# Performance work log

Measured on AMD Instinct MI355X. Metric: run time of the kernel, lower is better.

## Reference

```python
import jax, jax.numpy as jnp
import numpy as np

LAMBDA_COORD = 5.0
LAMBDA_NOOBJ = 0.5
GRID = 7
IMG = 448.0
CELL = IMG / GRID  # 64.0
EPS = 1e-06


def setup_inputs() -> dict:
    key = jax.random.key(0)
    k1, k2, k3 = jax.random.split(key, 3)
    B = 16384
    # predictions in [0.05, 1) so sqrt(w), sqrt(h) are well-behaved (as in training)
    input_ = jax.random.uniform(k1, (B, 30, GRID, GRID), dtype=jnp.float32, minval=0.05, maxval=1.0)
    target = jax.random.uniform(k2, (B, GRID, GRID, 30), dtype=jnp.float32, minval=0.05, maxval=1.0)
    # objectness target must be exactly 1.0 for 'has object' cells (code tests == 1)
    has_obj = (jax.random.uniform(k3, (B, GRID, GRID)) > 0.7).astype(jnp.float32)
    target = target.at[:, :, :, 4].set(has_obj)
    return {"input_": input_, "target": target}


def _corners(rows30, col, row):
    # rows30: [N,30] cell-relative preds; col/row: [N] grid indices
    # returns x1,y1,x2,y2 each [N,2] (two boxes per cell), clipped to image
    cx = rows30[:, jnp.array([0, 5])] * CELL + (col * CELL)[:, None]
    cy = rows30[:, jnp.array([1, 6])] * CELL + (row * CELL)[:, None]
    w = rows30[:, jnp.array([2, 7])] * IMG
    h = rows30[:, jnp.array([3, 8])] * IMG
    x1 = jnp.clip(cx - w / 2, 0.0, IMG)
    y1 = jnp.clip(cy - h / 2, 0.0, IMG)
    x2 = jnp.clip(cx + w / 2, 0.0, IMG)
    y2 = jnp.clip(cy + h / 2, 0.0, IMG)
    return x1, y1, x2, y2


def _yolo_loss(input_, target):
    B = input_.shape[0]
    # [B,30,7,7] -> [B,7,7,30] -> [N,30]
    x = jnp.transpose(input_, (0, 2, 3, 1)).reshape(-1, 30)
    t = target.reshape(-1, 30)
    N = x.shape[0]

    # grid offsets: flat index = b*49 + row*7 + col
    cell_idx = jnp.arange(GRID * GRID)
    col = jnp.tile((cell_idx % GRID).astype(x.dtype), B)  # [N]
    row = jnp.tile((cell_idx // GRID).astype(x.dtype), B)  # [N]

    ix1, iy1, ix2, iy2 = _corners(x, col, row)
    tx1, ty1, tx2, ty2 = _corners(t, col, row)

    # IoU of each predicted box vs same-slot target box, [N,2]
    iw = jnp.maximum(jnp.minimum(ix2, tx2) - jnp.maximum(ix1, tx1), EPS)
    ih = jnp.maximum(jnp.minimum(iy2, ty2) - jnp.maximum(iy1, ty1), EPS)
    inter = iw * ih
    area_sum = (ix2 - ix1) * (iy2 - iy1) + (tx2 - tx1) * (ty2 - ty1)
    iou2 = inter / (area_sum - inter)  # [N,2]

    m = iou2[:, 0] < iou2[:, 1]                       # box 1 selected where True
    iou = jnp.where(m, iou2[:, 1], iou2[:, 0])        # [N]

    has_obj = (t[:, 4] == 1.0).astype(x.dtype)        # [N]
    no_obj = 1.0 - has_obj

    sel = jnp.where(m[:, None], x[:, 5:10], x[:, :5])  # [N,5] selected box

    coordinate_error = jnp.sum(has_obj * ((sel[:, 0] - t[:, 0]) ** 2 + (sel[:, 1] - t[:, 1]) ** 2))
    size_error = jnp.sum(has_obj * ((jnp.sqrt(sel[:, 2]) - jnp.sqrt(t[:, 2])) ** 2
                                    + (jnp.sqrt(sel[:, 3]) - jnp.sqrt(t[:, 3])) ** 2))
    confidence_error = jnp.sum(has_obj * (sel[:, 4] - iou) ** 2)
    classification_error = jnp.sum(has_obj[:, None] * (x[:, 10:] - t[:, 10:]) ** 2)
    noobj_confidence_error = jnp.sum(no_obj * (x[:, 4] ** 2 + x[:, 9] ** 2))

    loss = (LAMBDA_COORD * coordinate_error + LAMBDA_COORD * size_error
            + confidence_error + LAMBDA_NOOBJ * noobj_confidence_error
            + classification_error)
    return loss / B


def reference(input_, target):
    return _yolo_loss(input_, target)
```

## Files before the change

kernel.cpp:

```cpp
#include <hip/hip_runtime.h>


#define CELLF   64.0f
#define IMGF    448.0f
#define EPSF    1e-6f
#define LAMBDA_COORD 5.0f
#define LAMBDA_NOOBJ 0.5f

__global__ __launch_bounds__(256) void yolo_loss_kernel(
    const float* __restrict__ input,
    const float* __restrict__ target,
    float* __restrict__ out,
    int ncells, float inv_b)
{
    __shared__ float s_t[256 * 30];
    __shared__ float s_part[4];

    const int tid  = threadIdx.x;
    const int base = blockIdx.x * 256;
    const int cells_here = min(256, ncells - base);

    if (cells_here == 256) {
        const float4* tg4 = reinterpret_cast<const float4*>(target + (size_t)base * 30);
        float4* s4 = reinterpret_cast<float4*>(s_t);
        #pragma unroll
        for (int i = 0; i < 8; ++i) {
            int idx = tid + i * 256;
            if (idx < 1920) s4[idx] = tg4[idx];
        }
    } else {
        int nflt = cells_here * 30;
        for (int i = tid; i < nflt; i += 256)
            s_t[i] = target[(size_t)base * 30 + i];
    }
    __syncthreads();

    float lv = 0.0f;
    const int n = base + tid;
    if (tid < cells_here) {
        const int b    = n / 49;
        const int cell = n - b * 49;
        const int row  = cell / 7;
        const int col  = cell - row * 7;

        const float* xin = input + (size_t)b * 1470 + cell;
        float x[30];
        #pragma unroll
        for (int c = 0; c < 30; ++c) x[c] = xin[c * 49];

        const float* t = s_t + tid * 30;

        const float colf = (float)col * CELLF;
        const float rowf = (float)row * CELLF;

        float iou[2];
        #pragma unroll
        for (int k = 0; k < 2; ++k) {
            const int o = 5 * k;
            float pcx = x[o + 0] * CELLF + colf;
            float pcy = x[o + 1] * CELLF + rowf;
            float pw  = x[o + 2] * IMGF;
            float ph  = x[o + 3] * IMGF;
            float px1 = fminf(fmaxf(pcx - 0.5f * pw, 0.0f), IMGF);
            float py1 = fminf(fmaxf(pcy - 0.5f * ph, 0.0f), IMGF);
            float px2 = fminf(fmaxf(pcx + 0.5f * pw, 0.0f), IMGF);
            float py2 = fminf(fmaxf(pcy + 0.5f * ph, 0.0f), IMGF);

            float tcx = t[o + 0] * CELLF + colf;
            float tcy = t[o + 1] * CELLF + rowf;
            float tw  = t[o + 2] * IMGF;
            float th  = t[o + 3] * IMGF;
            float tx1 = fminf(fmaxf(tcx - 0.5f * tw, 0.0f), IMGF);
            float ty1 = fminf(fmaxf(tcy - 0.5f * th, 0.0f), IMGF);
            float tx2 = fminf(fmaxf(tcx + 0.5f * tw, 0.0f), IMGF);
            float ty2 = fminf(fmaxf(tcy + 0.5f * th, 0.0f), IMGF);

            float iw = fmaxf(fminf(px2, tx2) - fmaxf(px1, tx1), EPSF);
            float ih = fmaxf(fminf(py2, ty2) - fmaxf(py1, ty1), EPSF);
            float inter = iw * ih;
            float area  = (px2 - px1) * (py2 - py1) + (tx2 - tx1) * (ty2 - ty1);
            iou[k] = inter / (area - inter);
        }

        const bool  m      = iou[0] < iou[1];
        const float iouSel = m ? iou[1] : iou[0];
        const float has_obj = (t[4] == 1.0f) ? 1.0f : 0.0f;
        const float no_obj  = 1.0f - has_obj;

        const float s0 = m ? x[5] : x[0];
        const float s1 = m ? x[6] : x[1];
        const float s2 = m ? x[7] : x[2];
        const float s3 = m ? x[8] : x[3];
        const float s4 = m ? x[9] : x[4];

        float d0 = s0 - t[0], d1 = s1 - t[1];
        float coord_e = d0 * d0 + d1 * d1;

        float e2 = sqrtf(s2) - sqrtf(t[2]);
        float e3 = sqrtf(s3) - sqrtf(t[3]);
        float size_e = e2 * e2 + e3 * e3;

        float dc = s4 - iouSel;
        float conf_e = dc * dc;

        float cls_e = 0.0f;
        #pragma unroll
        for (int c = 10; c < 30; ++c) {
            float d = x[c] - t[c];
            cls_e += d * d;
        }

        float noobj_e = x[4] * x[4] + x[9] * x[9];

        lv = has_obj * (LAMBDA_COORD * coord_e + LAMBDA_COORD * size_e + conf_e + cls_e)
           + LAMBDA_NOOBJ * no_obj * noobj_e;
    }

    float v = lv;
    #pragma unroll
    for (int off = 32; off > 0; off >>= 1)
        v += __shfl_down(v, off, 64);

    if ((tid & 63) == 0) s_part[tid >> 6] = v;
    __syncthreads();

    if (tid == 0) {
        float tot = s_part[0] + s_part[1] + s_part[2] + s_part[3];
        atomicAdd(out, tot * inv_b);
    }
}

extern "C" void kernel_launch(void* const* d_in, const int* in_sizes, int n_in,
                              void* d_out, int out_size, void* d_ws, size_t ws_size,
                              hipStream_t stream) {
    const float* input  = (const float*)d_in[0];
    const float* target = (const float*)d_in[1];
    float* out = (float*)d_out;

    const int B = in_sizes[0] / (30 * 49);
    const int ncells = B * 49;
    const int nblocks = (ncells + 255) / 256;

    hipMemsetAsync(out, 0, sizeof(float) * out_size, stream);
    yolo_loss_kernel<<<nblocks, 256, 0, stream>>>(input, target, out, ncells,
                                                  1.0f / (float)B);
}
```

Before: 207.6 us.

## Drop LDS target staging, process two cells per thread, two-pass reduction

```diff
diff --git a/kernel.cpp b/kernel.cpp
--- a/kernel.cpp
+++ b/kernel.cpp
@@ -7,127 +7,149 @@
 #define LAMBDA_COORD 5.0f
 #define LAMBDA_NOOBJ 0.5f
 
-__global__ __launch_bounds__(256) void yolo_loss_kernel(
+#define TPB 256
+#define CPT 2
+#define CPB (TPB * CPT)
+
+__device__ __forceinline__ float cell_loss(const float* __restrict__ input,
+                                           const float* __restrict__ target,
+                                           int n)
+{
+    const int b    = n / 49;
+    const int cell = n - b * 49;
+    const int row  = cell / 7;
+    const int col  = cell - row * 7;
+
+    const float* xin = input + (size_t)b * 1470 + cell;
+    float x[30];
+    #pragma unroll
+    for (int c = 0; c < 30; ++c) x[c] = xin[c * 49];
+
+    const float2* tp = reinterpret_cast<const float2*>(target + (size_t)n * 30);
+    float t[30];
+    #pragma unroll
+    for (int j = 0; j < 15; ++j) {
+        float2 v = tp[j];
+        t[2 * j]     = v.x;
+        t[2 * j + 1] = v.y;
+    }
+
+    const float colf = (float)col * CELLF;
+    const float rowf = (float)row * CELLF;
+
+    float iou[2];
+    #pragma unroll
+    for (int k = 0; k < 2; ++k) {
+        const int o = 5 * k;
+        float pcx = x[o + 0] * CELLF + colf;
+        float pcy = x[o + 1] * CELLF + rowf;
+        float pw  = x[o + 2] * IMGF;
+        float ph  = x[o + 3] * IMGF;
+        float px1 = fminf(fmaxf(pcx - 0.5f * pw, 0.0f), IMGF);
+        float py1 = fminf(fmaxf(pcy - 0.5f * ph, 0.0f), IMGF);
+        float px2 = fminf(fmaxf(pcx + 0.5f * pw, 0.0f), IMGF);
+        float py2 = fminf(fmaxf(pcy + 0.5f * ph, 0.0f), IMGF);
+
+        float tcx = t[o + 0] * CELLF + colf;
+        float tcy = t[o + 1] * CELLF + rowf;
+        float tw  = t[o + 2] * IMGF;
+        float th  = t[o + 3] * IMGF;
+        float tx1 = fminf(fmaxf(tcx - 0.5f * tw, 0.0f), IMGF);
+        float ty1 = fminf(fmaxf(tcy - 0.5f * th, 0.0f), IMGF);
+        float tx2 = fminf(fmaxf(tcx + 0.5f * tw, 0.0f), IMGF);
+        float ty2 = fminf(fmaxf(tcy + 0.5f * th, 0.0f), IMGF);
+
+        float iw = fmaxf(fminf(px2, tx2) - fmaxf(px1, tx1), EPSF);
+        float ih = fmaxf(fminf(py2, ty2) - fmaxf(py1, ty1), EPSF);
+        float inter = iw * ih;
+        float area  = (px2 - px1) * (py2 - py1) + (tx2 - tx1) * (ty2 - ty1);
+        iou[k] = inter / (area - inter);
+    }
+
+    const bool  m      = iou[0] < iou[1];
+    const float iouSel = m ? iou[1] : iou[0];
+    const float has_obj = (t[4] == 1.0f) ? 1.0f : 0.0f;
+    const float no_obj  = 1.0f - has_obj;
+
+    const float s0 = m ? x[5] : x[0];
+    const float s1 = m ? x[6] : x[1];
+    const float s2 = m ? x[7] : x[2];
+    const float s3 = m ? x[8] : x[3];
+    const float s4 = m ? x[9] : x[4];
+
+    float d0 = s0 - t[0], d1 = s1 - t[1];
+    float coord_e = d0 * d0 + d1 * d1;
+
+    float e2 = sqrtf(s2) - sqrtf(t[2]);
+    float e3 = sqrtf(s3) - sqrtf(t[3]);
+    float size_e = e2 * e2 + e3 * e3;
+
+    float dc = s4 - iouSel;
+    float conf_e = dc * dc;
+
+    float cls_e = 0.0f;
+    #pragma unroll
+    for (int c = 10; c < 30; ++c) {
+        float d = x[c] - t[c];
+        cls_e += d * d;
+    }
+
+    float noobj_e = x[4] * x[4] + x[9] * x[9];
+
+    return has_obj * (LAMBDA_COORD * coord_e + LAMBDA_COORD * size_e + conf_e + cls_e)
+         + LAMBDA_NOOBJ * no_obj * noobj_e;
+}
+
+__global__ __launch_bounds__(TPB) void yolo_main(
     const float* __restrict__ input,
     const float* __restrict__ target,
-    float* __restrict__ out,
-    int ncells, float inv_b)
+    float* __restrict__ partial,
+    int ncells)
 {
-    __shared__ float s_t[256 * 30];
-    __shared__ float s_part[4];
+    const int tid  = threadIdx.x;
+    const int base = blockIdx.x * CPB;
 
-    const int tid  = threadIdx.x;
-    const int base = blockIdx.x * 256;
-    const int cells_here = min(256, ncells - base);
+    float acc = 0.0f;
+    #pragma unroll
+    for (int it = 0; it < CPT; ++it) {
+        const int n = base + it * TPB + tid;
+        if (n < ncells) acc += cell_loss(input, target, n);
+    }
 
-    if (cells_here == 256) {
-        const float4* tg4 = reinterpret_cast<const float4*>(target + (size_t)base * 30);
-        float4* s4 = reinterpret_cast<float4*>(s_t);
-        #pragma unroll
-        for (int i = 0; i < 8; ++i) {
-            int idx = tid + i * 256;
-            if (idx < 1920) s4[idx] = tg4[idx];
-        }
-    } else {
-        int nflt = cells_here * 30;
-        for (int i = tid; i < nflt; i += 256)
-            s_t[i] = target[(size_t)base * 30 + i];
-    }
+    #pragma unroll
+    for (int off = 32; off > 0; off >>= 1)
+        acc += __shfl_down(acc, off, 64);
+
+    __shared__ float s_part[TPB / 64];
+    if ((tid & 63) == 0) s_part[tid >> 6] = acc;
     __syncthreads();
 
-    float lv = 0.0f;
-    const int n = base + tid;
-    if (tid < cells_here) {
-        const int b    = n / 49;
-        const int cell = n - b * 49;
-        const int row  = cell / 7;
-        const int col  = cell - row * 7;
+    if (tid == 0) {
+        float tot = 0.0f;
+        #pragma unroll
+        for (int w = 0; w < TPB / 64; ++w) tot += s_part[w];
+        partial[blockIdx.x] = tot;
+    }
+}
 
-        const float* xin = input + (size_t)b * 1470 + cell;
-        float x[30];
-        #pragma unroll
-        for (int c = 0; c < 30; ++c) x[c] = xin[c * 49];
+__global__ __launch_bounds__(256) void yolo_reduce(
+    const float* __restrict__ partial, int nparts,
+    float* __restrict__ out, float inv_b)
+{
+    const int tid = threadIdx.x;
+    float v = 0.0f;
+    for (int i = tid; i < nparts; i += 256) v += partial[i];
 
-        const float* t = s_t + tid * 30;
-
-        const float colf = (float)col * CELLF;
-        const float rowf = (float)row * CELLF;
-
-        float iou[2];
-        #pragma unroll
-        for (int k = 0; k < 2; ++k) {
-            const int o = 5 * k;
-            float pcx = x[o + 0] * CELLF + colf;
-            float pcy = x[o + 1] * CELLF + rowf;
-            float pw  = x[o + 2] * IMGF;
-            float ph  = x[o + 3] * IMGF;
-            float px1 = fminf(fmaxf(pcx - 0.5f * pw, 0.0f), IMGF);
-            float py1 = fminf(fmaxf(pcy - 0.5f * ph, 0.0f), IMGF);
-            float px2 = fminf(fmaxf(pcx + 0.5f * pw, 0.0f), IMGF);
-            float py2 = fminf(fmaxf(pcy + 0.5f * ph, 0.0f), IMGF);
-
-            float tcx = t[o + 0] * CELLF + colf;
-            float tcy = t[o + 1] * CELLF + rowf;
-            float tw  = t[o + 2] * IMGF;
-            float th  = t[o + 3] * IMGF;
-            float tx1 = fminf(fmaxf(tcx - 0.5f * tw, 0.0f), IMGF);
-            float ty1 = fminf(fmaxf(tcy - 0.5f * th, 0.0f), IMGF);
-            float tx2 = fminf(fmaxf(tcx + 0.5f * tw, 0.0f), IMGF);
-            float ty2 = fminf(fmaxf(tcy + 0.5f * th, 0.0f), IMGF);
-
-            float iw = fmaxf(fminf(px2, tx2) - fmaxf(px1, tx1), EPSF);
-            float ih = fmaxf(fminf(py2, ty2) - fmaxf(py1, ty1), EPSF);
-            float inter = iw * ih;
-            float area  = (px2 - px1) * (py2 - py1) + (tx2 - tx1) * (ty2 - ty1);
-            iou[k] = inter / (area - inter);
-        }
-
-        const bool  m      = iou[0] < iou[1];
-        const float iouSel = m ? iou[1] : iou[0];
-        const float has_obj = (t[4] == 1.0f) ? 1.0f : 0.0f;
-        const float no_obj  = 1.0f - has_obj;
-
-        const float s0 = m ? x[5] : x[0];
-        const float s1 = m ? x[6] : x[1];
-        const float s2 = m ? x[7] : x[2];
-        const float s3 = m ? x[8] : x[3];
-        const float s4 = m ? x[9] : x[4];
-
-        float d0 = s0 - t[0], d1 = s1 - t[1];
-        float coord_e = d0 * d0 + d1 * d1;
-
-        float e2 = sqrtf(s2) - sqrtf(t[2]);
-        float e3 = sqrtf(s3) - sqrtf(t[3]);
-        float size_e = e2 * e2 + e3 * e3;
-
-        float dc = s4 - iouSel;
-        float conf_e = dc * dc;
-
-        float cls_e = 0.0f;
-        #pragma unroll
-        for (int c = 10; c < 30; ++c) {
-            float d = x[c] - t[c];
-            cls_e += d * d;
-        }
-
-        float noobj_e = x[4] * x[4] + x[9] * x[9];
-
-        lv = has_obj * (LAMBDA_COORD * coord_e + LAMBDA_COORD * size_e + conf_e + cls_e)
-           + LAMBDA_NOOBJ * no_obj * noobj_e;
-    }
-
-    float v = lv;
     #pragma unroll
     for (int off = 32; off > 0; off >>= 1)
         v += __shfl_down(v, off, 64);
 
+    __shared__ float s_part[4];
     if ((tid & 63) == 0) s_part[tid >> 6] = v;
     __syncthreads();
 
-    if (tid == 0) {
-        float tot = s_part[0] + s_part[1] + s_part[2] + s_part[3];
-        atomicAdd(out, tot * inv_b);
-    }
+    if (tid == 0)
+        out[0] = (s_part[0] + s_part[1] + s_part[2] + s_part[3]) * inv_b;
 }
 
 extern "C" void kernel_launch(void* const* d_in, const int* in_sizes, int n_in,
@@ -136,12 +158,12 @@
     const float* input  = (const float*)d_in[0];
     const float* target = (const float*)d_in[1];
     float* out = (float*)d_out;
+    float* partial = (float*)d_ws;
 
     const int B = in_sizes[0] / (30 * 49);
     const int ncells = B * 49;
-    const int nblocks = (ncells + 255) / 256;
+    const int nblocks = (ncells + CPB - 1) / CPB;
 
-    hipMemsetAsync(out, 0, sizeof(float) * out_size, stream);
-    yolo_loss_kernel<<<nblocks, 256, 0, stream>>>(input, target, out, ncells,
-                                                  1.0f / (float)B);
+    yolo_main<<<nblocks, TPB, 0, stream>>>(input, target, partial, ncells);
+    yolo_reduce<<<1, 256, 0, stream>>>(partial, nblocks, out, 1.0f / (float)B);
 }
```

New measurement: 215.3 us. 3.7% more time.
